# Performance work log

Measured on AMD Instinct MI355X. Metric: run time of the kernel, lower is better.

Reference implementation:

```python
import jax, jax.numpy as jnp
import numpy as np

N_NODES = 100000
N_EDGES = 1600000
N_GRAPHS = 64
D_IN = 128
D_HID = 128
PERM = 128
N_CLS = 8


def _sage_conv(h, src, dst, W_self, W_neigh, b, n_nodes):
    # DGL SAGEConv 'mean': fc_self(h) + fc_neigh(mean of in-neighbor feats) + bias
    agg = jax.ops.segment_sum(h[src], dst, num_segments=n_nodes)          # [N, d]
    deg = jax.ops.segment_sum(jnp.ones((src.shape[0],), h.dtype), dst,
                              num_segments=n_nodes)                        # [N]
    mean = agg / jnp.maximum(deg, 1.0)[:, None]                            # zero-deg nodes -> 0
    return h @ W_self + mean @ W_neigh + b


def setup_inputs() -> dict:
    key = jax.random.key(0)
    ks = jax.random.split(key, 12)
    s = 1.0 / np.sqrt(D_IN)
    inp = {
        'h': jax.random.normal(ks[0], (N_NODES, D_IN), jnp.float32),
        'perm_features': jax.random.normal(ks[1], (N_GRAPHS, PERM), jnp.float32),
        'src': jax.random.randint(ks[2], (N_EDGES,), 0, N_NODES),
        'dst': jax.random.randint(ks[3], (N_EDGES,), 0, N_NODES),
        'graph_ids': jnp.sort(jax.random.randint(ks[4], (N_NODES,), 0, N_GRAPHS)),
        'W1_self': jax.random.normal(ks[5], (D_IN, D_HID), jnp.float32) * s,
        'W1_neigh': jax.random.normal(ks[6], (D_IN, D_HID), jnp.float32) * s,
        'b1': jnp.zeros((D_HID,), jnp.float32),
        'W2_self': jax.random.normal(ks[7], (D_HID, D_HID), jnp.float32) * s,
        'W2_neigh': jax.random.normal(ks[8], (D_HID, D_HID), jnp.float32) * s,
        'b2': jnp.zeros((D_HID,), jnp.float32),
        'Wc': jax.random.normal(ks[9], (D_HID + PERM, N_CLS), jnp.float32) * s,
        'bc': jnp.zeros((N_CLS,), jnp.float32),
    }
    return inp


def reference(h, perm_features, src, dst, graph_ids,
              W1_self, W1_neigh, b1, W2_self, W2_neigh, b2, Wc, bc):
    n = h.shape[0]
    h1 = jax.nn.relu(_sage_conv(h, src, dst, W1_self, W1_neigh, b1, n))
    h2 = _sage_conv(h1, src, dst, W2_self, W2_neigh, b2, n)
    # dgl.mean_nodes: per-graph mean of node features
    gsum = jax.ops.segment_sum(h2, graph_ids, num_segments=N_GRAPHS)       # [B, d]
    gcnt = jax.ops.segment_sum(jnp.ones((n,), h.dtype), graph_ids,
                               num_segments=N_GRAPHS)                       # [B]
    hg = gsum / jnp.maximum(gcnt, 1.0)[:, None]
    combined = jnp.concatenate([hg, perm_features], axis=1)                 # [B, d+perm]
    return combined @ Wc + bc
```

## Files before the change

kernel.cpp:

```cpp
#include <hip/hip_runtime.h>

#define DID 128
#define NCLS 8
#define NPB 512
#define NPB_SHIFT 9
#define NBLK 512
#define CAP 12288
#define PCHUNK 64

typedef __attribute__((ext_vector_type(8))) short bf16x8;
typedef __attribute__((ext_vector_type(4))) float f32x4;
typedef __attribute__((ext_vector_type(8))) unsigned short u16x8;

static __device__ __forceinline__ unsigned short f2bf(float f) {
  union { float f; unsigned int u; } x;
  x.f = f;
  unsigned int r = (x.u + 0x7fffu + ((x.u >> 16) & 1u)) >> 16;
  return (unsigned short)r;
}
static __device__ __forceinline__ float bfhi(unsigned int v) {
  union { unsigned int u; float f; } x;
  x.u = v & 0xffff0000u;
  return x.f;
}
static __device__ __forceinline__ float bflo(unsigned int v) {
  union { unsigned int u; float f; } x;
  x.u = v << 16;
  return x.f;
}

__global__ __launch_bounds__(256) void kB_hist(const int* __restrict__ dst,
                                               int* __restrict__ hist, int E,
                                               int nbuk) {
  __shared__ int c[256];
  int tid = threadIdx.x;
  for (int i = tid; i < nbuk; i += 256) c[i] = 0;
  __syncthreads();
  int epb = (E + NBLK - 1) / NBLK;
  int e0 = blockIdx.x * epb;
  int e1 = min(E, e0 + epb);
  for (int e = e0 + tid; e < e1; e += 256)
    atomicAdd(&c[dst[e] >> NPB_SHIFT], 1);
  __syncthreads();
  for (int i = tid; i < nbuk; i += 256)
    hist[(size_t)i * NBLK + blockIdx.x] = c[i];
}

__global__ void k_scan1(const int* __restrict__ deg, int* __restrict__ rp,
                        int* __restrict__ part, int n) {
  __shared__ int sd[256];
  int t = threadIdx.x;
  int base = blockIdx.x * 1024 + t * 4;
  int v0 = (base + 0 < n) ? deg[base + 0] : 0;
  int v1 = (base + 1 < n) ? deg[base + 1] : 0;
  int v2 = (base + 2 < n) ? deg[base + 2] : 0;
  int v3 = (base + 3 < n) ? deg[base + 3] : 0;
  int ts = v0 + v1 + v2 + v3;
  sd[t] = ts;
  __syncthreads();
  for (int off = 1; off < 256; off <<= 1) {
    int x = 0;
    if (t >= off) x = sd[t - off];
    __syncthreads();
    if (t >= off) sd[t] += x;
    __syncthreads();
  }
  int excl = sd[t] - ts;
  if (base + 0 < n) rp[base + 0] = excl;
  if (base + 1 < n) rp[base + 1] = excl + v0;
  if (base + 2 < n) rp[base + 2] = excl + v0 + v1;
  if (base + 3 < n) rp[base + 3] = excl + v0 + v1 + v2;
  if (t == 255) part[blockIdx.x] = sd[255];
}

__global__ void k_scan2(int* __restrict__ part, int nblk) {
  __shared__ int sd[1024];
  int t = threadIdx.x;
  int v = (t < nblk) ? part[t] : 0;
  sd[t] = v;
  __syncthreads();
  for (int off = 1; off < 1024; off <<= 1) {
    int x = 0;
    if (t >= off) x = sd[t - off];
    __syncthreads();
    if (t >= off) sd[t] += x;
    __syncthreads();
  }
  if (t < nblk) part[t] = sd[t] - v;
}

__global__ void k_scan3(int* __restrict__ rp, const int* __restrict__ part,
                        int n, int E) {
  int t = threadIdx.x;
  int add = part[blockIdx.x];
  int base = blockIdx.x * 1024 + t * 4;
#pragma unroll
  for (int i = 0; i < 4; ++i)
    if (base + i < n) rp[base + i] += add;
  if (blockIdx.x == 0 && t == 0) rp[n] = E;
}

__global__ __launch_bounds__(256) void kB_scat(const int* __restrict__ src,
                                               const int* __restrict__ dst,
                                               const int* __restrict__ off,
                                               unsigned long long* __restrict__ pairs,
                                               int E, int nbuk) {
  __shared__ int cur[256];
  int tid = threadIdx.x;
  for (int i = tid; i < nbuk; i += 256)
    cur[i] = off[(size_t)i * NBLK + blockIdx.x];
  __syncthreads();
  int epb = (E + NBLK - 1) / NBLK;
  int e0 = blockIdx.x * epb;
  int e1 = min(E, e0 + epb);
  for (int e = e0 + tid; e < e1; e += 256) {
    int s = src[e];
    int d = dst[e];
    int p = atomicAdd(&cur[d >> NPB_SHIFT], 1);
    pairs[p] = ((unsigned long long)(unsigned)d << 32) | (unsigned)s;
  }
}

__global__ __launch_bounds__(512) void kB_build(
    const unsigned long long* __restrict__ pairs, const int* __restrict__ off,
    int* __restrict__ rp, int* __restrict__ col, int N, int nbuk, int E) {
  __shared__ int cnt[NPB];
  __shared__ int exc[NPB];
  __shared__ int colstage[CAP];
  int tid = threadIdx.x;
  int b = blockIdx.x;
  int eb = off[(size_t)b * NBLK];
  int ee = off[(size_t)(b + 1) * NBLK];
  int m = ee - eb;

  cnt[tid] = 0;
  __syncthreads();
  for (int i = eb + tid; i < ee; i += NPB) {
    int d = (int)(pairs[i] >> 32);
    atomicAdd(&cnt[d & (NPB - 1)], 1);
  }
  __syncthreads();
  exc[tid] = cnt[tid];
  __syncthreads();
  for (int o = 1; o < NPB; o <<= 1) {
    int v = (tid >= o) ? exc[tid - o] : 0;
    __syncthreads();
    exc[tid] += v;
    __syncthreads();
  }
  int myexc = exc[tid] - cnt[tid];
  int node = b * NPB + tid;
  if (node < N) rp[node] = eb + myexc;
  if (b == nbuk - 1 && tid == 0) rp[N] = E;
  __syncthreads();
  cnt[tid] = myexc;
  __syncthreads();
  if (m <= CAP) {
    for (int i = eb + tid; i < ee; i += NPB) {
      unsigned long long pr = pairs[i];
      int d = (int)(pr >> 32);
      int s = (int)(pr & 0xffffffffu);
      int p = atomicAdd(&cnt[d & (NPB - 1)], 1);
      colstage[p] = s;
    }
    __syncthreads();
    for (int i = tid; i < m; i += NPB) col[eb + i] = colstage[i];
  } else {
    for (int i = eb + tid; i < ee; i += NPB) {
      unsigned long long pr = pairs[i];
      int d = (int)(pr >> 32);
      int s = (int)(pr & 0xffffffffu);
      int p = atomicAdd(&cnt[d & (NPB - 1)], 1);
      col[eb + p] = s;
    }
  }
}

__global__ void k_h2b(const float* __restrict__ h, unsigned short* __restrict__ hb,
                      int total8) {
  int i = blockIdx.x * 256 + threadIdx.x;
  if (i >= total8) return;
  const float4* h4 = (const float4*)h;
  float4 a = h4[(size_t)i * 2];
  float4 b = h4[(size_t)i * 2 + 1];
  u16x8 o;
  o[0] = f2bf(a.x); o[1] = f2bf(a.y); o[2] = f2bf(a.z); o[3] = f2bf(a.w);
  o[4] = f2bf(b.x); o[5] = f2bf(b.y); o[6] = f2bf(b.z); o[7] = f2bf(b.w);
  *(u16x8*)(hb + (size_t)i * 8) = o;
}

__global__ void k_pack4(const float* __restrict__ W0, const float* __restrict__ W1,
                        const float* __restrict__ W2, const float* __restrict__ W3,
                        unsigned short* __restrict__ P0, unsigned short* __restrict__ P1,
                        unsigned short* __restrict__ P2, unsigned short* __restrict__ P3) {
  int gid = blockIdx.x * 256 + threadIdx.x;
  int m = gid >> 14;
  int idx = gid & 16383;
  int j = idx & 7;
  int l = (idx >> 3) & 63;
  int kf = (idx >> 9) & 3;
  int ct = idx >> 11;
  int colc = ct * 16 + (l & 15);
  int k = kf * 32 + (l >> 4) * 8 + j;
  const float* W = (m == 0) ? W0 : (m == 1) ? W1 : (m == 2) ? W2 : W3;
  unsigned short* P = (m == 0) ? P0 : (m == 1) ? P1 : (m == 2) ? P2 : P3;
  P[idx] = f2bf(W[k * 128 + colc]);
}

__global__ __launch_bounds__(256, 2) void k_gemm2(
    const unsigned short* __restrict__ hb, const unsigned short* __restrict__ WpS,
    const unsigned short* __restrict__ WpN, float* __restrict__ z,
    unsigned short* __restrict__ yb, int n) {
  const int l = threadIdx.x & 63;
  const int w = threadIdx.x >> 6;
  const int rowW = blockIdx.x * 128 + w * 32;
  const int cl = l & 15;
  const int cg = l >> 4;

  bf16x8 A[2][4];
#pragma unroll
  for (int rt = 0; rt < 2; ++rt) {
    int row = rowW + rt * 16 + cl;
#pragma unroll
    for (int kf = 0; kf < 4; ++kf) {
      if (row < n)
        A[rt][kf] = *(const bf16x8*)(hb + (size_t)row * 128 + kf * 32 + cg * 8);
      else
        A[rt][kf] = (bf16x8){0, 0, 0, 0, 0, 0, 0, 0};
    }
  }

  f32x4 accS[2][8], accN[2][8];
#pragma unroll
  for (int rt = 0; rt < 2; ++rt)
#pragma unroll
    for (int ct = 0; ct < 8; ++ct) {
      accS[rt][ct] = (f32x4){0.f, 0.f, 0.f, 0.f};
      accN[rt][ct] = (f32x4){0.f, 0.f, 0.f, 0.f};
    }

#pragma unroll
  for (int ct = 0; ct < 8; ++ct) {
    bf16x8 BS[4], BN[4];
#pragma unroll
    for (int kf = 0; kf < 4; ++kf) {
      BS[kf] = *(const bf16x8*)(WpS + ((ct * 4 + kf) * 64 + l) * 8);
      BN[kf] = *(const bf16x8*)(WpN + ((ct * 4 + kf) * 64 + l) * 8);
    }
#pragma unroll
    for (int rt = 0; rt < 2; ++rt)
#pragma unroll
      for (int kf = 0; kf < 4; ++kf) {
        accS[rt][ct] =
            __builtin_amdgcn_mfma_f32_16x16x32_bf16(A[rt][kf], BS[kf], accS[rt][ct], 0, 0, 0);
        accN[rt][ct] =
            __builtin_amdgcn_mfma_f32_16x16x32_bf16(A[rt][kf], BN[kf], accN[rt][ct], 0, 0, 0);
      }
  }

#pragma unroll
  for (int rt = 0; rt < 2; ++rt)
#pragma unroll
    for (int ct = 0; ct < 8; ++ct) {
#pragma unroll
      for (int r = 0; r < 4; ++r) {
        int row = rowW + rt * 16 + cg * 4 + r;
        if (row < n) {
          int colc = ct * 16 + cl;
          z[(size_t)row * 128 + colc] = accS[rt][ct][r];
          yb[(size_t)row * 128 + colc] = f2bf(accN[rt][ct][r]);
        }
      }
    }
}

template <int OUTMODE>
__global__ __launch_bounds__(256, 8) void k_aggr2(
    const unsigned int* __restrict__ Y, const float* Z,
    const int* __restrict__ rp, const int* __restrict__ col,
    const float* __restrict__ bias, void* outp, int n) {
  int wid = (blockIdx.x * 256 + threadIdx.x) >> 6;
  int lane = threadIdx.x & 63;
  if (wid >= n) return;
  int s = rp[wid], e = rp[wid + 1];
  float ax = 0.f, ay = 0.f;
  int i = s;
  for (; i + 8 <= e; i += 8) {
    unsigned int v0 = Y[(size_t)col[i + 0] * 64 + lane];
    unsigned int v1 = Y[(size_t)col[i + 1] * 64 + lane];
    unsigned int v2 = Y[(size_t)col[i + 2] * 64 + lane];
    unsigned int v3 = Y[(size_t)col[i + 3] * 64 + lane];
    unsigned int v4 = Y[(size_t)col[i + 4] * 64 + lane];
    unsigned int v5 = Y[(size_t)col[i + 5] * 64 + lane];
    unsigned int v6 = Y[(size_t)col[i + 6] * 64 + lane];
    unsigned int v7 = Y[(size_t)col[i + 7] * 64 + lane];
    ax += bflo(v0) + bflo(v1) + bflo(v2) + bflo(v3) + bflo(v4) + bflo(v5) +
          bflo(v6) + bflo(v7);
    ay += bfhi(v0) + bfhi(v1) + bfhi(v2) + bfhi(v3) + bfhi(v4) + bfhi(v5) +
          bfhi(v6) + bfhi(v7);
  }
  for (; i + 4 <= e; i += 4) {
    unsigned int v0 = Y[(size_t)col[i + 0] * 64 + lane];
    unsigned int v1 = Y[(size_t)col[i + 1] * 64 + lane];
    unsigned int v2 = Y[(size_t)col[i + 2] * 64 + lane];
    unsigned int v3 = Y[(size_t)col[i + 3] * 64 + lane];
    ax += bflo(v0) + bflo(v1) + bflo(v2) + bflo(v3);
    ay += bfhi(v0) + bfhi(v1) + bfhi(v2) + bfhi(v3);
  }
  for (; i < e; ++i) {
    unsigned int v = Y[(size_t)col[i] * 64 + lane];
    ax += bflo(v);
    ay += bfhi(v);
  }
  int deg = e - s;
  float scale = 1.0f / (float)(deg > 1 ? deg : 1);
  float2 zv = ((const float2*)Z)[(size_t)wid * 64 + lane];
  float2 bb = ((const float2*)bias)[lane];
  float ox = zv.x + ax * scale + bb.x;
  float oy = zv.y + ay * scale + bb.y;
  if (OUTMODE == 1) {
    ox = fmaxf(ox, 0.f);
    oy = fmaxf(oy, 0.f);
    unsigned int packed = (unsigned int)f2bf(ox) | ((unsigned int)f2bf(oy) << 16);
    ((unsigned int*)outp)[(size_t)wid * 64 + lane] = packed;
  } else {
    ((float2*)outp)[(size_t)wid * 64 + lane] = make_float2(ox, oy);
  }
}

__global__ void k_bounds(const int* __restrict__ gids, int* __restrict__ gs,
                         int n, int NG) {
  int g = threadIdx.x;
  if (g < NG) {
    int lo = 0, hi = n;
    while (lo < hi) {
      int m = (lo + hi) >> 1;
      if (gids[m] < g) lo = m + 1;
      else hi = m;
    }
    gs[g] = lo;
  } else if (g == NG) {
    gs[NG] = n;
  }
}

__global__ __launch_bounds__(256) void k_pool(const float* __restrict__ H2,
                                              const int* __restrict__ gs,
                                              float* __restrict__ gsum, int NG) {
  int g = blockIdx.x / PCHUNK;
  int c = blockIdx.x % PCHUNK;
  int t = threadIdx.x;
  int s = gs[g], e = gs[g + 1];
  int cnt = e - s;
  int per = (cnt + PCHUNK - 1) / PCHUNK;
  int rs = s + c * per;
  int re = rs + per < e ? rs + per : e;
  if (rs >= re) return;
  int rslot = t >> 5;
  int d4 = t & 31;
  const float4* H4 = (const float4*)H2;
  float4 acc = make_float4(0.f, 0.f, 0.f, 0.f);
  for (int r = rs + rslot; r < re; r += 8) {
    float4 v = H4[(size_t)r * 32 + d4];
    acc.x += v.x; acc.y += v.y; acc.z += v.z; acc.w += v.w;
  }
  __shared__ float4 sacc[256];
  sacc[t] = acc;
  __syncthreads();
#pragma unroll
  for (int o = 4; o >= 1; o >>= 1) {
    if (rslot < o) {
      float4 a = sacc[t];
      float4 b = sacc[t + o * 32];
      a.x += b.x; a.y += b.y; a.z += b.z; a.w += b.w;
      sacc[t] = a;
    }
    __syncthreads();
  }
  if (t < 32) {
    float4 a = sacc[t];
    atomicAdd(&gsum[g * DID + t * 4 + 0], a.x);
    atomicAdd(&gsum[g * DID + t * 4 + 1], a.y);
    atomicAdd(&gsum[g * DID + t * 4 + 2], a.z);
    atomicAdd(&gsum[g * DID + t * 4 + 3], a.w);
  }
}

__global__ void k_head(const float* __restrict__ gsum,
                       const float* __restrict__ perm,
                       const float* __restrict__ Wc,
                       const float* __restrict__ bc,
                       const int* __restrict__ gs, float* __restrict__ out,
                       int NG) {
  int t = threadIdx.x;
  if (t >= NG * NCLS) return;
  int g = t >> 3, c = t & 7;
  int cnt = gs[g + 1] - gs[g];
  float inv = 1.0f / (float)(cnt > 1 ? cnt : 1);
  float acc = bc[c];
#pragma unroll 4
  for (int k = 0; k < DID; ++k)
    acc += gsum[g * DID + k] * inv * Wc[k * NCLS + c];
#pragma unroll 4
  for (int k = 0; k < DID; ++k)
    acc += perm[g * DID + k] * Wc[(DID + k) * NCLS + c];
  out[g * NCLS + c] = acc;
}

extern "C" void kernel_launch(void* const* d_in, const int* in_sizes, int n_in,
                              void* d_out, int out_size, void* d_ws,
                              size_t ws_size, hipStream_t stream) {
  const float* h = (const float*)d_in[0];
  const float* perm = (const float*)d_in[1];
  const int* src = (const int*)d_in[2];
  const int* dst = (const int*)d_in[3];
  const int* gids = (const int*)d_in[4];
  const float* W1s = (const float*)d_in[5];
  const float* W1n = (const float*)d_in[6];
  const float* b1 = (const float*)d_in[7];
  const float* W2s = (const float*)d_in[8];
  const float* W2n = (const float*)d_in[9];
  const float* b2 = (const float*)d_in[10];
  const float* Wc = (const float*)d_in[11];
  const float* bc = (const float*)d_in[12];
  float* out = (float*)d_out;

  const int N = in_sizes[0] / DID;
  const int E = in_sizes[2];
  const int NG = in_sizes[1] / DID;
  const int nbuk = (N + NPB - 1) >> NPB_SHIFT;
  const int nscan = nbuk * NBLK;

  char* w = (char*)d_ws;
  size_t off_ = 0;
  auto alloc = [&](size_t bytes) -> void* {
    off_ = (off_ + 511) & ~(size_t)511;
    void* p = w + off_;
    off_ += bytes;
    return p;
  };
  float* gsum = (float*)alloc((size_t)NG * DID * 4);
  size_t zbytes = off_;
  int* hist = (int*)alloc((size_t)nscan * 4);
  int* boff = (int*)alloc((size_t)(nscan + 1) * 4);
  int* part = (int*)alloc(1024 * 4);
  int* rp = (int*)alloc((size_t)(N + 1) * 4);
  int* gs = (int*)alloc((size_t)(NG + 1) * 4);
  int* col = (int*)alloc((size_t)E * 4);
  unsigned long long* pairs = (unsigned long long*)alloc((size_t)E * 8);
  unsigned short* hb = (unsigned short*)alloc((size_t)N * DID * 2);
  unsigned short* yb = (unsigned short*)alloc((size_t)N * DID * 2);
  float* z = (float*)alloc((size_t)N * DID * 4);
  unsigned short* Wp1s = (unsigned short*)alloc(128 * 128 * 2);
  unsigned short* Wp1n = (unsigned short*)alloc(128 * 128 * 2);
  unsigned short* Wp2s = (unsigned short*)alloc(128 * 128 * 2);
  unsigned short* Wp2n = (unsigned short*)alloc(128 * 128 * 2);

  hipMemsetAsync(d_ws, 0, zbytes, stream);

  const int nchunk = (nscan + 1023) / 1024;
  const int ngb = (N + 127) / 128;
  const int nagg = (N + 3) / 4;
  const int ncvt = ((N * DID / 8) + 255) / 256;

  k_h2b<<<ncvt, 256, 0, stream>>>(h, hb, N * DID / 8);
  k_pack4<<<256, 256, 0, stream>>>(W1s, W1n, W2s, W2n, Wp1s, Wp1n, Wp2s, Wp2n);

  kB_hist<<<NBLK, 256, 0, stream>>>(dst, hist, E, nbuk);
  k_scan1<<<nchunk, 256, 0, stream>>>(hist, boff, part, nscan);
  k_scan2<<<1, 1024, 0, stream>>>(part, nchunk);
  k_scan3<<<nchunk, 256, 0, stream>>>(boff, part, nscan, E);
  kB_scat<<<NBLK, 256, 0, stream>>>(src, dst, boff, pairs, E, nbuk);
  kB_build<<<nbuk, NPB, 0, stream>>>(pairs, boff, rp, col, N, nbuk, E);

  k_gemm2<<<ngb, 256, 0, stream>>>(hb, Wp1s, Wp1n, z, yb, N);
  k_aggr2<1><<<nagg, 256, 0, stream>>>((const unsigned int*)yb, z, rp, col, b1,
                                       (void*)hb, N);

  k_gemm2<<<ngb, 256, 0, stream>>>(hb, Wp2s, Wp2n, z, yb, N);
  k_aggr2<0><<<nagg, 256, 0, stream>>>((const unsigned int*)yb, z, rp, col, b2,
                                       (void*)z, N);

  k_bounds<<<1, 128, 0, stream>>>(gids, gs, N, NG);
  k_pool<<<NG * PCHUNK, 256, 0, stream>>>(z, gs, gsum, NG);
  k_head<<<1, 512, 0, stream>>>(gsum, perm, Wc, bc, gs, out, NG);
}
```

Baseline: 415.2 us.

## Fuse prep kernels into one launch and widen aggregation gathers to 8 bytes

Merges the bf16 conversion of h, the weight packing, the dst histogram and the gsum zeroing into a single block-partitioned k_prep kernel. This removes the memset, the separate k_bounds launch and several other launches. The aggregation kernel now splits each wave into two half-waves that each gather a different neighbor row with 8-byte loads. The halves are combined with a cross-half shuffle, which doubles gather width per instruction but lowers the occupancy hint from 8 to 4 blocks. Pool and head now recompute graph bounds by binary search per block, adding some redundant work.

```diff
diff --git a/kernel.cpp b/kernel.cpp
--- a/kernel.cpp
+++ b/kernel.cpp
@@ -28,22 +28,66 @@
   x.u = v << 16;
   return x.f;
 }
-
-__global__ __launch_bounds__(256) void kB_hist(const int* __restrict__ dst,
-                                               int* __restrict__ hist, int E,
-                                               int nbuk) {
+static __device__ __forceinline__ int lowerb(const int* __restrict__ a, int n,
+                                             int key) {
+  int lo = 0, hi = n;
+  while (lo < hi) {
+    int m = (lo + hi) >> 1;
+    if (a[m] < key) lo = m + 1;
+    else hi = m;
+  }
+  return lo;
+}
+
+__global__ __launch_bounds__(256) void k_prep(
+    const float* __restrict__ h, unsigned short* __restrict__ hb, int total8,
+    int ncvt, const float* __restrict__ W0, const float* __restrict__ W1,
+    const float* __restrict__ W2, const float* __restrict__ W3,
+    unsigned short* __restrict__ P0, unsigned short* __restrict__ P1,
+    unsigned short* __restrict__ P2, unsigned short* __restrict__ P3,
+    const int* __restrict__ dst, int* __restrict__ hist, int E, int nbuk,
+    float* __restrict__ gsum, int ngsum) {
   __shared__ int c[256];
+  int bid = blockIdx.x;
   int tid = threadIdx.x;
-  for (int i = tid; i < nbuk; i += 256) c[i] = 0;
-  __syncthreads();
-  int epb = (E + NBLK - 1) / NBLK;
-  int e0 = blockIdx.x * epb;
-  int e1 = min(E, e0 + epb);
-  for (int e = e0 + tid; e < e1; e += 256)
-    atomicAdd(&c[dst[e] >> NPB_SHIFT], 1);
-  __syncthreads();
-  for (int i = tid; i < nbuk; i += 256)
-    hist[(size_t)i * NBLK + blockIdx.x] = c[i];
+  if (bid < ncvt) {
+    int i = bid * 256 + tid;
+    if (i >= total8) return;
+    const float4* h4 = (const float4*)h;
+    float4 a = h4[(size_t)i * 2];
+    float4 b = h4[(size_t)i * 2 + 1];
+    u16x8 o;
+    o[0] = f2bf(a.x); o[1] = f2bf(a.y); o[2] = f2bf(a.z); o[3] = f2bf(a.w);
+    o[4] = f2bf(b.x); o[5] = f2bf(b.y); o[6] = f2bf(b.z); o[7] = f2bf(b.w);
+    *(u16x8*)(hb + (size_t)i * 8) = o;
+  } else if (bid < ncvt + 256) {
+    int gid = (bid - ncvt) * 256 + tid;
+    int m = gid >> 14;
+    int idx = gid & 16383;
+    int j = idx & 7;
+    int l = (idx >> 3) & 63;
+    int kf = (idx >> 9) & 3;
+    int ct = idx >> 11;
+    int colc = ct * 16 + (l & 15);
+    int k = kf * 32 + (l >> 4) * 8 + j;
+    const float* W = (m == 0) ? W0 : (m == 1) ? W1 : (m == 2) ? W2 : W3;
+    unsigned short* P = (m == 0) ? P0 : (m == 1) ? P1 : (m == 2) ? P2 : P3;
+    P[idx] = f2bf(W[k * 128 + colc]);
+  } else if (bid < ncvt + 256 + NBLK) {
+    int b = bid - ncvt - 256;
+    for (int i = tid; i < nbuk; i += 256) c[i] = 0;
+    __syncthreads();
+    int epb = (E + NBLK - 1) / NBLK;
+    int e0 = b * epb;
+    int e1 = min(E, e0 + epb);
+    for (int e = e0 + tid; e < e1; e += 256)
+      atomicAdd(&c[dst[e] >> NPB_SHIFT], 1);
+    __syncthreads();
+    for (int i = tid; i < nbuk; i += 256)
+      hist[(size_t)i * NBLK + b] = c[i];
+  } else {
+    for (int i = tid; i < ngsum; i += 256) gsum[i] = 0.f;
+  }
 }
 
 __global__ void k_scan1(const int* __restrict__ deg, int* __restrict__ rp,
@@ -176,37 +220,6 @@
   }
 }
 
-__global__ void k_h2b(const float* __restrict__ h, unsigned short* __restrict__ hb,
-                      int total8) {
-  int i = blockIdx.x * 256 + threadIdx.x;
-  if (i >= total8) return;
-  const float4* h4 = (const float4*)h;
-  float4 a = h4[(size_t)i * 2];
-  float4 b = h4[(size_t)i * 2 + 1];
-  u16x8 o;
-  o[0] = f2bf(a.x); o[1] = f2bf(a.y); o[2] = f2bf(a.z); o[3] = f2bf(a.w);
-  o[4] = f2bf(b.x); o[5] = f2bf(b.y); o[6] = f2bf(b.z); o[7] = f2bf(b.w);
-  *(u16x8*)(hb + (size_t)i * 8) = o;
-}
-
-__global__ void k_pack4(const float* __restrict__ W0, const float* __restrict__ W1,
-                        const float* __restrict__ W2, const float* __restrict__ W3,
-                        unsigned short* __restrict__ P0, unsigned short* __restrict__ P1,
-                        unsigned short* __restrict__ P2, unsigned short* __restrict__ P3) {
-  int gid = blockIdx.x * 256 + threadIdx.x;
-  int m = gid >> 14;
-  int idx = gid & 16383;
-  int j = idx & 7;
-  int l = (idx >> 3) & 63;
-  int kf = (idx >> 9) & 3;
-  int ct = idx >> 11;
-  int colc = ct * 16 + (l & 15);
-  int k = kf * 32 + (l >> 4) * 8 + j;
-  const float* W = (m == 0) ? W0 : (m == 1) ? W1 : (m == 2) ? W2 : W3;
-  unsigned short* P = (m == 0) ? P0 : (m == 1) ? P1 : (m == 2) ? P2 : P3;
-  P[idx] = f2bf(W[k * 128 + colc]);
-}
-
 __global__ __launch_bounds__(256, 2) void k_gemm2(
     const unsigned short* __restrict__ hb, const unsigned short* __restrict__ WpS,
     const unsigned short* __restrict__ WpN, float* __restrict__ z,
@@ -275,82 +288,74 @@
 }
 
 template <int OUTMODE>
-__global__ __launch_bounds__(256, 8) void k_aggr2(
+__global__ __launch_bounds__(256, 4) void k_aggr2(
     const unsigned int* __restrict__ Y, const float* Z,
     const int* __restrict__ rp, const int* __restrict__ col,
     const float* __restrict__ bias, void* outp, int n) {
   int wid = (blockIdx.x * 256 + threadIdx.x) >> 6;
   int lane = threadIdx.x & 63;
   if (wid >= n) return;
+  int half = lane >> 5;
+  int hl = lane & 31;
+  const uint2* __restrict__ Y2 = (const uint2*)Y;
   int s = rp[wid], e = rp[wid + 1];
-  float ax = 0.f, ay = 0.f;
+  float a0 = 0.f, a1 = 0.f, a2 = 0.f, a3 = 0.f;
   int i = s;
-  for (; i + 8 <= e; i += 8) {
-    unsigned int v0 = Y[(size_t)col[i + 0] * 64 + lane];
-    unsigned int v1 = Y[(size_t)col[i + 1] * 64 + lane];
-    unsigned int v2 = Y[(size_t)col[i + 2] * 64 + lane];
-    unsigned int v3 = Y[(size_t)col[i + 3] * 64 + lane];
-    unsigned int v4 = Y[(size_t)col[i + 4] * 64 + lane];
-    unsigned int v5 = Y[(size_t)col[i + 5] * 64 + lane];
-    unsigned int v6 = Y[(size_t)col[i + 6] * 64 + lane];
-    unsigned int v7 = Y[(size_t)col[i + 7] * 64 + lane];
-    ax += bflo(v0) + bflo(v1) + bflo(v2) + bflo(v3) + bflo(v4) + bflo(v5) +
-          bflo(v6) + bflo(v7);
-    ay += bfhi(v0) + bfhi(v1) + bfhi(v2) + bfhi(v3) + bfhi(v4) + bfhi(v5) +
-          bfhi(v6) + bfhi(v7);
-  }
-  for (; i + 4 <= e; i += 4) {
-    unsigned int v0 = Y[(size_t)col[i + 0] * 64 + lane];
-    unsigned int v1 = Y[(size_t)col[i + 1] * 64 + lane];
-    unsigned int v2 = Y[(size_t)col[i + 2] * 64 + lane];
-    unsigned int v3 = Y[(size_t)col[i + 3] * 64 + lane];
-    ax += bflo(v0) + bflo(v1) + bflo(v2) + bflo(v3);
-    ay += bfhi(v0) + bfhi(v1) + bfhi(v2) + bfhi(v3);
-  }
-  for (; i < e; ++i) {
-    unsigned int v = Y[(size_t)col[i] * 64 + lane];
-    ax += bflo(v);
-    ay += bfhi(v);
-  }
+  for (; i + 16 <= e; i += 16) {
+#pragma unroll
+    for (int k = 0; k < 8; ++k) {
+      int c = col[i + 2 * k + half];
+      uint2 v = Y2[(size_t)c * 32 + hl];
+      a0 += bflo(v.x); a1 += bfhi(v.x);
+      a2 += bflo(v.y); a3 += bfhi(v.y);
+    }
+  }
+  if (i < e) {
+#pragma unroll
+    for (int k = 0; k < 8; ++k) {
+      int idx = i + 2 * k + half;
+      if (idx < e) {
+        int c = col[idx];
+        uint2 v = Y2[(size_t)c * 32 + hl];
+        a0 += bflo(v.x); a1 += bfhi(v.x);
+        a2 += bflo(v.y); a3 += bfhi(v.y);
+      }
+    }
+  }
+  a0 += __shfl_xor(a0, 32);
+  a1 += __shfl_xor(a1, 32);
+  a2 += __shfl_xor(a2, 32);
+  a3 += __shfl_xor(a3, 32);
   int deg = e - s;
   float scale = 1.0f / (float)(deg > 1 ? deg : 1);
-  float2 zv = ((const float2*)Z)[(size_t)wid * 64 + lane];
-  float2 bb = ((const float2*)bias)[lane];
-  float ox = zv.x + ax * scale + bb.x;
-  float oy = zv.y + ay * scale + bb.y;
-  if (OUTMODE == 1) {
-    ox = fmaxf(ox, 0.f);
-    oy = fmaxf(oy, 0.f);
-    unsigned int packed = (unsigned int)f2bf(ox) | ((unsigned int)f2bf(oy) << 16);
-    ((unsigned int*)outp)[(size_t)wid * 64 + lane] = packed;
-  } else {
-    ((float2*)outp)[(size_t)wid * 64 + lane] = make_float2(ox, oy);
-  }
-}
-
-__global__ void k_bounds(const int* __restrict__ gids, int* __restrict__ gs,
-                         int n, int NG) {
-  int g = threadIdx.x;
-  if (g < NG) {
-    int lo = 0, hi = n;
-    while (lo < hi) {
-      int m = (lo + hi) >> 1;
-      if (gids[m] < g) lo = m + 1;
-      else hi = m;
-    }
-    gs[g] = lo;
-  } else if (g == NG) {
-    gs[NG] = n;
+  if (half == 0) {
+    float4 zv = ((const float4*)Z)[(size_t)wid * 32 + hl];
+    float4 bb = ((const float4*)bias)[hl];
+    float o0 = zv.x + a0 * scale + bb.x;
+    float o1 = zv.y + a1 * scale + bb.y;
+    float o2 = zv.z + a2 * scale + bb.z;
+    float o3 = zv.w + a3 * scale + bb.w;
+    if (OUTMODE == 1) {
+      o0 = fmaxf(o0, 0.f); o1 = fmaxf(o1, 0.f);
+      o2 = fmaxf(o2, 0.f); o3 = fmaxf(o3, 0.f);
+      uint2 p;
+      p.x = (unsigned)f2bf(o0) | ((unsigned)f2bf(o1) << 16);
+      p.y = (unsigned)f2bf(o2) | ((unsigned)f2bf(o3) << 16);
+      ((uint2*)outp)[(size_t)wid * 32 + hl] = p;
+    } else {
+      ((float4*)outp)[(size_t)wid * 32 + hl] = make_float4(o0, o1, o2, o3);
+    }
   }
 }
 
 __global__ __launch_bounds__(256) void k_pool(const float* __restrict__ H2,
-                                              const int* __restrict__ gs,
-                                              float* __restrict__ gsum, int NG) {
+                                              const int* __restrict__ gids,
+                                              float* __restrict__ gsum, int N) {
   int g = blockIdx.x / PCHUNK;
   int c = blockIdx.x % PCHUNK;
   int t = threadIdx.x;
-  int s = gs[g], e = gs[g + 1];
+  int s = lowerb(gids, N, g);
+  int e = lowerb(gids, N, g + 1);
   int cnt = e - s;
   int per = (cnt + PCHUNK - 1) / PCHUNK;
   int rs = s + c * per;
@@ -390,12 +395,12 @@
                        const float* __restrict__ perm,
                        const float* __restrict__ Wc,
                        const float* __restrict__ bc,
-                       const int* __restrict__ gs, float* __restrict__ out,
-                       int NG) {
+                       const int* __restrict__ gids, float* __restrict__ out,
+                       int N, int NG) {
   int t = threadIdx.x;
   if (t >= NG * NCLS) return;
   int g = t >> 3, c = t & 7;
-  int cnt = gs[g + 1] - gs[g];
+  int cnt = lowerb(gids, N, g + 1) - lowerb(gids, N, g);
   float inv = 1.0f / (float)(cnt > 1 ? cnt : 1);
   float acc = bc[c];
 #pragma unroll 4
@@ -440,12 +445,10 @@
     return p;
   };
   float* gsum = (float*)alloc((size_t)NG * DID * 4);
-  size_t zbytes = off_;
   int* hist = (int*)alloc((size_t)nscan * 4);
   int* boff = (int*)alloc((size_t)(nscan + 1) * 4);
   int* part = (int*)alloc(1024 * 4);
   int* rp = (int*)alloc((size_t)(N + 1) * 4);
-  int* gs = (int*)alloc((size_t)(NG + 1) * 4);
   int* col = (int*)alloc((size_t)E * 4);
   unsigned long long* pairs = (unsigned long long*)alloc((size_t)E * 8);
   unsigned short* hb = (unsigned short*)alloc((size_t)N * DID * 2);
@@ -456,17 +459,16 @@
   unsigned short* Wp2s = (unsigned short*)alloc(128 * 128 * 2);
   unsigned short* Wp2n = (unsigned short*)alloc(128 * 128 * 2);
 
-  hipMemsetAsync(d_ws, 0, zbytes, stream);
-
   const int nchunk = (nscan + 1023) / 1024;
   const int ngb = (N + 127) / 128;
   const int nagg = (N + 3) / 4;
-  const int ncvt = ((N * DID / 8) + 255) / 256;
-
-  k_h2b<<<ncvt, 256, 0, stream>>>(h, hb, N * DID / 8);
-  k_pack4<<<256, 256, 0, stream>>>(W1s, W1n, W2s, W2n, Wp1s, Wp1n, Wp2s, Wp2n);
-
-  kB_hist<<<NBLK, 256, 0, stream>>>(dst, hist, E, nbuk);
+  const int total8 = N * DID / 8;
+  const int ncvt = (total8 + 255) / 256;
+
+  k_prep<<<ncvt + 256 + NBLK + 1, 256, 0, stream>>>(
+      h, hb, total8, ncvt, W1s, W1n, W2s, W2n, Wp1s, Wp1n, Wp2s, Wp2n, dst,
+      hist, E, nbuk, gsum, NG * DID);
+
   k_scan1<<<nchunk, 256, 0, stream>>>(hist, boff, part, nscan);
   k_scan2<<<1, 1024, 0, stream>>>(part, nchunk);
   k_scan3<<<nchunk, 256, 0, stream>>>(boff, part, nscan, E);
@@ -481,7 +483,6 @@
   k_aggr2<0><<<nagg, 256, 0, stream>>>((const unsigned int*)yb, z, rp, col, b2,
                                        (void*)z, N);
 
-  k_bounds<<<1, 128, 0, stream>>>(gids, gs, N, NG);
-  k_pool<<<NG * PCHUNK, 256, 0, stream>>>(z, gs, gsum, NG);
-  k_head<<<1, 512, 0, stream>>>(gsum, perm, Wc, bc, gs, out, NG);
-}
+  k_pool<<<NG * PCHUNK, 256, 0, stream>>>(z, gids, gsum, N);
+  k_head<<<1, 512, 0, stream>>>(gsum, perm, Wc, bc, gids, out, N, NG);
+}
```

Measured after the change: 441.6 us. 1.06x slower.
